# Kernel tuning notes

Hardware: AMD Instinct MI355X
Metric: run time of the kernel (lower is better)

Reference implementation:

```python
import jax, jax.numpy as jnp
import numpy as np

Q_MAX = 127.0  # 2**(8-1) - 1

def _quant_per_tensor_absmax(t):
    # scale = clamp(absmax, 1e-5) / 127 ; q = round(t / scale)
    scale = jnp.maximum(jnp.max(jnp.abs(t)), 1e-5) / Q_MAX
    q = jnp.round(t / scale)
    return q, scale

def setup_inputs() -> dict:
    key = jax.random.key(0)
    k1, k2, k3 = jax.random.split(key, 3)
    B, S, IN, OUT = 4, 2048, 4096, 4096
    x = jax.random.normal(k1, (B, S, IN), dtype=jnp.float32)
    weight = jax.random.normal(k2, (OUT, IN), dtype=jnp.float32)
    bias = jax.random.normal(k3, (1, OUT), dtype=jnp.float32)
    return {"x": x, "weight": weight, "bias": bias}

def reference(x, weight, bias):
    # per-tensor weight quantization (done at from_float time in the original)
    q_w, s_w = _quant_per_tensor_absmax(weight)   # q_w: [OUT, IN] integer-valued
    # per-tensor activation quantization (forward path)
    q_x, s_x = _quant_per_tensor_absmax(x)        # q_x: [B, S, IN] integer-valued
    # int8 GEMM (simulated in fp32: values are small integers) + fused dequant
    y = jnp.einsum('bsi,oi->bso', q_x, q_w)       # [B, S, OUT]
    y = y * (s_x * s_w) + bias                    # dequant scale + bias
    return y
```

## Files before the change

kernel.cpp:

```cpp
#include <hip/hip_runtime.h>
#include <hip/hip_bf16.h>
#include <stdint.h>

#define M_DIM 8192
#define N_DIM 4096
#define K_DIM 4096

typedef int i32x4 __attribute__((ext_vector_type(4)));

#define NB_X 2048
#define NB_W 1024
#define NB_TOT (NB_X + NB_W)

__global__ void w8a8_absmax_kernel(const float* __restrict__ x,
                                   const float* __restrict__ w,
                                   float* __restrict__ partials) {
    int b = blockIdx.x;
    const float4* p;
    int n4, bi, nb;
    if (b < NB_X) { p = (const float4*)x; n4 = (M_DIM * K_DIM) / 4; bi = b;        nb = NB_X; }
    else          { p = (const float4*)w; n4 = (N_DIM * K_DIM) / 4; bi = b - NB_X; nb = NB_W; }

    float m = 0.f;
    int stride = nb * 256;
    for (int i = bi * 256 + threadIdx.x; i < n4; i += stride) {
        float4 v = p[i];
        m = fmaxf(m, fmaxf(fmaxf(fabsf(v.x), fabsf(v.y)), fmaxf(fabsf(v.z), fabsf(v.w))));
    }
    #pragma unroll
    for (int o = 32; o > 0; o >>= 1)
        m = fmaxf(m, __shfl_xor(m, o, 64));

    __shared__ float red[4];
    if ((threadIdx.x & 63) == 0) red[threadIdx.x >> 6] = m;
    __syncthreads();
    if (threadIdx.x == 0)
        partials[b] = fmaxf(fmaxf(red[0], red[1]), fmaxf(red[2], red[3]));
}

__global__ void w8a8_finalize_kernel(const float* __restrict__ partials,
                                     float* __restrict__ finals) {
    int base = (blockIdx.x == 0) ? 0 : NB_X;
    int n    = (blockIdx.x == 0) ? NB_X : NB_W;
    float m = 0.f;
    for (int i = threadIdx.x; i < n; i += 256)
        m = fmaxf(m, partials[base + i]);
    #pragma unroll
    for (int o = 32; o > 0; o >>= 1)
        m = fmaxf(m, __shfl_xor(m, o, 64));
    __shared__ float red[4];
    if ((threadIdx.x & 63) == 0) red[threadIdx.x >> 6] = m;
    __syncthreads();
    if (threadIdx.x == 0) {
        m = fmaxf(fmaxf(red[0], red[1]), fmaxf(red[2], red[3]));
        finals[blockIdx.x] = fmaxf(m, 1e-5f) / 127.0f;
    }
}

__global__ void w8a8_quant_kernel(const float* __restrict__ x,
                                  const float* __restrict__ w,
                                  unsigned* __restrict__ qx,
                                  unsigned* __restrict__ qw,
                                  const float* __restrict__ finals) {
    int b = blockIdx.x;
    const float4* in4;
    unsigned* outq;
    int n4, bi, nb;
    float scale;
    if (b < NB_X) { in4 = (const float4*)x; outq = qx; n4 = (M_DIM * K_DIM) / 4; bi = b;        nb = NB_X; scale = finals[0]; }
    else          { in4 = (const float4*)w; outq = qw; n4 = (N_DIM * K_DIM) / 4; bi = b - NB_X; nb = NB_W; scale = finals[1]; }

    int stride = nb * 256;
    for (int i = bi * 256 + threadIdx.x; i < n4; i += stride) {
        float4 v = in4[i];
        int q0 = (int)rintf(v.x / scale);
        int q1 = (int)rintf(v.y / scale);
        int q2 = (int)rintf(v.z / scale);
        int q3 = (int)rintf(v.w / scale);
        outq[i] = (unsigned)(q0 & 0xff) | ((unsigned)(q1 & 0xff) << 8) |
                  ((unsigned)(q2 & 0xff) << 16) | ((unsigned)(q3 & 0xff) << 24);
    }
}

#define BM 128
#define BN 128
#define BK 128
#define NTILES_N (N_DIM / BN)

__global__ __launch_bounds__(256, 4) void w8a8_gemm_kernel(
    const signed char* __restrict__ qa,
    const signed char* __restrict__ qb,
    const float* __restrict__ bias,
    const float* __restrict__ finals,
    float* __restrict__ out)
{
    __shared__ signed char As[BM * BK];
    __shared__ signed char Bs[BN * BK];

    float sprod = finals[0] * finals[1];

    int bid = blockIdx.x;
    int cpx = gridDim.x >> 3;
    int swz = (bid & 7) * cpx + (bid >> 3);
    int tm = swz / NTILES_N;
    int tn = swz % NTILES_N;

    int t = threadIdx.x;
    int lane = t & 63;
    int w = t >> 6;
    int wm = (w >> 1) * 64;
    int wn = (w & 1) * 64;
    int fr = lane & 15;
    int fg = lane >> 4;

    const signed char* a_base = qa + (size_t)tm * BM * K_DIM;
    const signed char* b_base = qb + (size_t)tn * BN * K_DIM;

    i32x4 acc[4][4] = {};

    for (int kt = 0; kt < K_DIM; kt += BK) {
        #pragma unroll
        for (int i = 0; i < 4; ++i) {
            int row = i * 32 + (t >> 3);
            int c = t & 7;
            int cs = c ^ (row & 7);
            const signed char* ga = a_base + (size_t)row * K_DIM + kt + cs * 16;
            const signed char* gb = b_base + (size_t)row * K_DIM + kt + cs * 16;
            __builtin_amdgcn_global_load_lds(
                (const __attribute__((address_space(1))) void*)ga,
                (__attribute__((address_space(3))) void*)(As + (i * 256 + t) * 16),
                16, 0, 0);
            __builtin_amdgcn_global_load_lds(
                (const __attribute__((address_space(1))) void*)gb,
                (__attribute__((address_space(3))) void*)(Bs + (i * 256 + t) * 16),
                16, 0, 0);
        }
        __syncthreads();

        #pragma unroll
        for (int kk = 0; kk < 2; ++kk) {
            i32x4 afrag[4], bfrag[4];
            #pragma unroll
            for (int m = 0; m < 4; ++m) {
                int r = wm + m * 16 + fr;
                int chunk = (kk * 4 + fg) ^ (r & 7);
                afrag[m] = *(const i32x4*)(As + r * BK + chunk * 16);
            }
            #pragma unroll
            for (int n = 0; n < 4; ++n) {
                int r = wn + n * 16 + fr;
                int chunk = (kk * 4 + fg) ^ (r & 7);
                bfrag[n] = *(const i32x4*)(Bs + r * BK + chunk * 16);
            }
            #pragma unroll
            for (int m = 0; m < 4; ++m)
                #pragma unroll
                for (int n = 0; n < 4; ++n)
                    acc[m][n] = __builtin_amdgcn_mfma_i32_16x16x64_i8(
                        afrag[m], bfrag[n], acc[m][n], 0, 0, 0);
        }
        __syncthreads();
    }

    int orow0 = tm * BM + wm + fg * 4;
    int ocol0 = tn * BN + wn + fr;
    #pragma unroll
    for (int n = 0; n < 4; ++n) {
        int col = ocol0 + n * 16;
        float bv = bias[col];
        #pragma unroll
        for (int m = 0; m < 4; ++m) {
            int row = orow0 + m * 16;
            #pragma unroll
            for (int r = 0; r < 4; ++r) {
                out[(size_t)(row + r) * N_DIM + col] = (float)acc[m][n][r] * sprod + bv;
            }
        }
    }
}

extern "C" void kernel_launch(void* const* d_in, const int* in_sizes, int n_in,
                              void* d_out, int out_size, void* d_ws, size_t ws_size,
                              hipStream_t stream) {
    const float* x    = (const float*)d_in[0];
    const float* wgt  = (const float*)d_in[1];
    const float* bias = (const float*)d_in[2];
    float* out = (float*)d_out;

    char* ws = (char*)d_ws;
    float* finals   = (float*)ws;
    float* partials = (float*)(ws + 256);
    signed char* qx = (signed char*)(ws + 16384);
    signed char* qw = qx + (size_t)M_DIM * K_DIM;

    w8a8_absmax_kernel<<<NB_TOT, 256, 0, stream>>>(x, wgt, partials);
    w8a8_finalize_kernel<<<2, 256, 0, stream>>>(partials, finals);
    w8a8_quant_kernel<<<NB_TOT, 256, 0, stream>>>(x, wgt, (unsigned*)qx, (unsigned*)qw, finals);
    w8a8_gemm_kernel<<<(M_DIM / BM) * (N_DIM / BN), 256, 0, stream>>>(qx, qw, bias, finals, out);
}
```

Measured before the change: 242.4 us.

## Rewrite int8 GEMM as 256x256 tile, 8-wave, double-buffered LDS pipeline

Replaces the 128x128 single-buffer GEMM with 256x256 tiles computed by 512 threads (8 waves), double-buffered LDS (128 KB), and an interleaved schedule. Each wave loads a quarter of its fragments, issues MFMAs under raised priority, and stages the next tile's global loads between compute phases, with vmcnt waits and raw barriers in place of __syncthreads. The goal is more data reuse per tile and overlapping global-to-LDS transfers with MFMA work. In exchange it uses more registers and LDS, so occupancy drops, and the loop runs past the last tile, issuing wrapped prefetches of the first tiles that are never used.

After: 226.4 us. 1.07x faster.

```diff
diff --git a/kernel.cpp b/kernel.cpp
--- a/kernel.cpp
+++ b/kernel.cpp
@@ -82,98 +82,162 @@
     }
 }
 
-#define BM 128
-#define BN 128
+#define BM 256
+#define BN 256
 #define BK 128
-#define NTILES_N (N_DIM / BN)
-
-__global__ __launch_bounds__(256, 4) void w8a8_gemm_kernel(
+#define NT (K_DIM / BK)
+#define NTN (N_DIM / BN)
+#define LDS_BUF 65536
+
+#define STAGE_A(BUF, MH, KT) do {                                              \
+    _Pragma("unroll")                                                          \
+    for (int r_ = 0; r_ < 2; ++r_)                                             \
+        __builtin_amdgcn_global_load_lds(                                      \
+            (const __attribute__((address_space(1))) void*)(a_base + (size_t)((KT) + goffA[MH][r_])), \
+            (__attribute__((address_space(3))) void*)(lds + (BUF)*LDS_BUF + (MH)*16384 + ldst[r_]),   \
+            16, 0, 0);                                                         \
+} while (0)
+
+#define STAGE_B(BUF, NH, KT) do {                                              \
+    _Pragma("unroll")                                                          \
+    for (int r_ = 0; r_ < 2; ++r_)                                             \
+        __builtin_amdgcn_global_load_lds(                                      \
+            (const __attribute__((address_space(1))) void*)(b_base + (size_t)((KT) + goffB[NH][r_])), \
+            (__attribute__((address_space(3))) void*)(lds + (BUF)*LDS_BUF + 32768 + (NH)*16384 + ldst[r_]), \
+            16, 0, 0);                                                         \
+} while (0)
+
+#define LOAD_A(BUF, MH) do {                                                   \
+    _Pragma("unroll")                                                          \
+    for (int m4_ = 0; m4_ < 4; ++m4_) {                                        \
+        aF[m4_][0] = *(const i32x4*)(lds + (BUF)*LDS_BUF + (MH)*16384 + laneA + m4_*2048 + koff[0]); \
+        aF[m4_][1] = *(const i32x4*)(lds + (BUF)*LDS_BUF + (MH)*16384 + laneA + m4_*2048 + koff[1]); \
+    }                                                                          \
+} while (0)
+
+#define LOAD_B(BUF, NH) do {                                                   \
+    _Pragma("unroll")                                                          \
+    for (int n1_ = 0; n1_ < 2; ++n1_) {                                        \
+        bF[n1_][0] = *(const i32x4*)(lds + (BUF)*LDS_BUF + 32768 + (NH)*16384 + laneB + n1_*2048 + koff[0]); \
+        bF[n1_][1] = *(const i32x4*)(lds + (BUF)*LDS_BUF + 32768 + (NH)*16384 + laneB + n1_*2048 + koff[1]); \
+    }                                                                          \
+} while (0)
+
+#define MMA(MH, NH) do {                                                       \
+    __builtin_amdgcn_s_setprio(1);                                             \
+    _Pragma("unroll")                                                          \
+    for (int m4_ = 0; m4_ < 4; ++m4_) {                                        \
+        _Pragma("unroll")                                                      \
+        for (int n1_ = 0; n1_ < 2; ++n1_) {                                    \
+            i32x4 c_ = acc[(MH)*4 + m4_][(NH)*2 + n1_];                        \
+            c_ = __builtin_amdgcn_mfma_i32_16x16x64_i8(aF[m4_][0], bF[n1_][0], c_, 0, 0, 0); \
+            c_ = __builtin_amdgcn_mfma_i32_16x16x64_i8(aF[m4_][1], bF[n1_][1], c_, 0, 0, 0); \
+            acc[(MH)*4 + m4_][(NH)*2 + n1_] = c_;                              \
+        }                                                                      \
+    }                                                                          \
+    __builtin_amdgcn_s_setprio(0);                                             \
+} while (0)
+
+#define BAR() __builtin_amdgcn_s_barrier()
+#define VMW8() asm volatile("s_waitcnt vmcnt(8)" ::: "memory")
+
+#define TILE_BODY(BUF, KT2) do {                                               \
+    LOAD_A(BUF, 0); LOAD_B(BUF, 0);                         \
+    BAR(); MMA(0, 0); BAR();                                                   \
+    LOAD_A(BUF, 1);                                         \
+    BAR(); MMA(1, 0); BAR();                                                   \
+    LOAD_B(BUF, 1);                                         \
+    STAGE_B(BUF, 0, KT2);                              \
+    BAR(); MMA(1, 1); BAR();                                                   \
+    LOAD_A(BUF, 0);                                         \
+    STAGE_A(BUF, 1, KT2);                              \
+    STAGE_B(BUF, 1, KT2);                              \
+    BAR(); MMA(0, 1); BAR();                                                   \
+    STAGE_A(BUF, 0, KT2);                              \
+    VMW8();                                   \
+    BAR();                                                                     \
+} while (0)
+
+__global__ __launch_bounds__(512, 2) void w8a8_gemm_kernel(
     const signed char* __restrict__ qa,
     const signed char* __restrict__ qb,
     const float* __restrict__ bias,
     const float* __restrict__ finals,
     float* __restrict__ out)
 {
-    __shared__ signed char As[BM * BK];
-    __shared__ signed char Bs[BN * BK];
-
-    float sprod = finals[0] * finals[1];
+    __shared__ __align__(16) char lds[2 * LDS_BUF];
+
+    int t    = threadIdx.x;
+    int lane = t & 63;
+    int wid  = t >> 6;
+    int wm   = wid >> 2;
+    int wn   = wid & 3;
+    int fr   = lane & 15;
+    int fg   = lane >> 4;
+    int frb2 = (fr >> 2) & 1;
 
     int bid = blockIdx.x;
     int cpx = gridDim.x >> 3;
     int swz = (bid & 7) * cpx + (bid >> 3);
-    int tm = swz / NTILES_N;
-    int tn = swz % NTILES_N;
-
-    int t = threadIdx.x;
-    int lane = t & 63;
-    int w = t >> 6;
-    int wm = (w >> 1) * 64;
-    int wn = (w & 1) * 64;
-    int fr = lane & 15;
-    int fg = lane >> 4;
+    int tm = swz / NTN;
+    int tn = swz % NTN;
 
     const signed char* a_base = qa + (size_t)tm * BM * K_DIM;
     const signed char* b_base = qb + (size_t)tn * BN * K_DIM;
 
-    i32x4 acc[4][4] = {};
-
-    for (int kt = 0; kt < K_DIM; kt += BK) {
-        #pragma unroll
-        for (int i = 0; i < 4; ++i) {
-            int row = i * 32 + (t >> 3);
-            int c = t & 7;
-            int cs = c ^ (row & 7);
-            const signed char* ga = a_base + (size_t)row * K_DIM + kt + cs * 16;
-            const signed char* gb = b_base + (size_t)row * K_DIM + kt + cs * 16;
-            __builtin_amdgcn_global_load_lds(
-                (const __attribute__((address_space(1))) void*)ga,
-                (__attribute__((address_space(3))) void*)(As + (i * 256 + t) * 16),
-                16, 0, 0);
-            __builtin_amdgcn_global_load_lds(
-                (const __attribute__((address_space(1))) void*)gb,
-                (__attribute__((address_space(3))) void*)(Bs + (i * 256 + t) * 16),
-                16, 0, 0);
-        }
-        __syncthreads();
-
-        #pragma unroll
-        for (int kk = 0; kk < 2; ++kk) {
-            i32x4 afrag[4], bfrag[4];
-            #pragma unroll
-            for (int m = 0; m < 4; ++m) {
-                int r = wm + m * 16 + fr;
-                int chunk = (kk * 4 + fg) ^ (r & 7);
-                afrag[m] = *(const i32x4*)(As + r * BK + chunk * 16);
-            }
-            #pragma unroll
-            for (int n = 0; n < 4; ++n) {
-                int r = wn + n * 16 + fr;
-                int chunk = (kk * 4 + fg) ^ (r & 7);
-                bfrag[n] = *(const i32x4*)(Bs + r * BK + chunk * 16);
-            }
-            #pragma unroll
-            for (int m = 0; m < 4; ++m)
-                #pragma unroll
-                for (int n = 0; n < 4; ++n)
-                    acc[m][n] = __builtin_amdgcn_mfma_i32_16x16x64_i8(
-                        afrag[m], bfrag[n], acc[m][n], 0, 0, 0);
-        }
-        __syncthreads();
-    }
-
-    int orow0 = tm * BM + wm + fg * 4;
-    int ocol0 = tn * BN + wn + fr;
+    int goffA[2][2], goffB[2][2], ldst[2];
+    #pragma unroll
+    for (int r = 0; r < 2; ++r) {
+        int unit = r * 512 + t;
+        int sl   = unit >> 3;
+        int c    = unit & 7;
+        int cs   = c ^ (sl & 7);
+        int rowA = (sl & 63) + ((sl >> 6) & 1) * 128;
+        goffA[0][r] = rowA * K_DIM + cs * 16;
+        goffA[1][r] = (rowA + 64) * K_DIM + cs * 16;
+        int rowB = ((sl >> 5) & 3) * 64 + (sl & 31);
+        goffB[0][r] = rowB * K_DIM + cs * 16;
+        goffB[1][r] = (rowB + 32) * K_DIM + cs * 16;
+        ldst[r] = r * 8192 + t * 16;
+    }
+
+    int laneA = (wm * 64 + fr) * 128 + (fg ^ (fr & 3)) * 16;
+    int laneB = (wn * 32 + fr) * 128 + (fg ^ (fr & 3)) * 16;
+    int koff[2];
+    koff[0] = frb2 * 64;
+    koff[1] = 64 - frb2 * 64;
+
+    i32x4 acc[8][4] = {};
+    i32x4 aF[4][2], bF[2][2];
+
+    STAGE_A(0, 0, 0);  STAGE_A(0, 1, 0);  STAGE_B(0, 0, 0);  STAGE_B(0, 1, 0);
+    STAGE_A(1, 0, BK); STAGE_A(1, 1, BK); STAGE_B(1, 0, BK); STAGE_B(1, 1, BK);
+    VMW8();
+    BAR();
+
+    #pragma unroll 1
+    for (int it = 0; it < NT / 2; ++it) {
+        int kt2 = ((2 * it + 2) & (NT - 1)) * BK;
+        int kt3 = ((2 * it + 3) & (NT - 1)) * BK;
+        TILE_BODY(0, kt2);
+        TILE_BODY(1, kt3);
+    }
+    asm volatile("s_waitcnt vmcnt(0)" ::: "memory");
+    BAR();
+
+    float sprod = finals[0] * finals[1];
+    int orow0 = tm * BM + wm * 128 + fg * 4;
+    int ocol0 = tn * BN + wn * 64 + fr;
     #pragma unroll
     for (int n = 0; n < 4; ++n) {
         int col = ocol0 + n * 16;
         float bv = bias[col];
         #pragma unroll
-        for (int m = 0; m < 4; ++m) {
+        for (int m = 0; m < 8; ++m) {
             int row = orow0 + m * 16;
             #pragma unroll
-            for (int r = 0; r < 4; ++r) {
-                out[(size_t)(row + r) * N_DIM + col] = (float)acc[m][n][r] * sprod + bv;
+            for (int rr = 0; rr < 4; ++rr) {
+                out[(size_t)(row + rr) * N_DIM + col] = (float)acc[m][n][rr] * sprod + bv;
             }
         }
     }
@@ -196,5 +260,5 @@
     w8a8_absmax_kernel<<<NB_TOT, 256, 0, stream>>>(x, wgt, partials);
     w8a8_finalize_kernel<<<2, 256, 0, stream>>>(partials, finals);
     w8a8_quant_kernel<<<NB_TOT, 256, 0, stream>>>(x, wgt, (unsigned*)qx, (unsigned*)qw, finals);
-    w8a8_gemm_kernel<<<(M_DIM / BM) * (N_DIM / BN), 256, 0, stream>>>(qx, qw, bias, finals, out);
-}
+    w8a8_gemm_kernel<<<(M_DIM / BM) * (N_DIM / BN), 512, 0, stream>>>(qx, qw, bias, finals, out);
+}
```
